# Optimization experiments

Hardware: AMD Instinct MI355X
Metric: run time of the kernel (lower is better)

The kernel has to match this reference:

```python
import jax, jax.numpy as jnp
import numpy as np

B, T, C = 4, 2048, 1024
N_HEAD = 16
HEAD_DIM = C // N_HEAD


def setup_inputs() -> dict:
    key = jax.random.key(0)
    ks = jax.random.split(key, 5)
    s = 0.02
    return {
        "x": jax.random.normal(ks[0], (B, T, C), dtype=jnp.float32),
        "w_attn": jax.random.normal(ks[1], (C, 3 * C), dtype=jnp.float32) * s,
        "b_attn": jnp.zeros((3 * C,), dtype=jnp.float32),
        "w_proj": jax.random.normal(ks[2], (C, C), dtype=jnp.float32) * s,
        "b_proj": jnp.zeros((C,), dtype=jnp.float32),
    }


def reference(x, w_attn, b_attn, w_proj, b_proj):
    Bx, Tx, Cx = x.shape
    qkv = x @ w_attn + b_attn  # [B,T,3C]
    q, k, v = jnp.split(qkv, 3, axis=-1)
    # [B, H, T, D]
    q = q.reshape(Bx, Tx, N_HEAD, HEAD_DIM).transpose(0, 2, 1, 3)
    k = k.reshape(Bx, Tx, N_HEAD, HEAD_DIM).transpose(0, 2, 1, 3)
    v = v.reshape(Bx, Tx, N_HEAD, HEAD_DIM).transpose(0, 2, 1, 3)
    scale = 1.0 / np.sqrt(HEAD_DIM).astype(np.float32)
    att = jnp.einsum("bhqd,bhkd->bhqk", q, k) * scale  # [B,H,T,T]
    causal = jnp.tril(jnp.ones((Tx, Tx), dtype=bool))
    att = jnp.where(causal[None, None], att, jnp.float32(-jnp.inf))
    att = jax.nn.softmax(att, axis=-1)
    y = jnp.einsum("bhqk,bhkd->bhqd", att, v)  # [B,H,T,D]
    y = y.transpose(0, 2, 1, 3).reshape(Bx, Tx, Cx)
    return y @ w_proj + b_proj
```

## Files before the change

### kernel.cpp

```cpp
#include <hip/hip_runtime.h>
#include <hip/hip_bf16.h>

#define T_SEQ 2048
#define NHEAD 16
#define HDIM  64
#define CDIM  1024

typedef __attribute__((ext_vector_type(8))) short bf16x8;
typedef __attribute__((ext_vector_type(4))) short bf16x4;
typedef __attribute__((ext_vector_type(4))) float f32x4;

__device__ __forceinline__ unsigned short f2bf(float f) {
  union { __hip_bfloat16 h; unsigned short u; } c;
  c.h = __float2bfloat16(f);
  return c.u;
}

#define GLD16(g, l) __builtin_amdgcn_global_load_lds( \
  (const __attribute__((address_space(1))) void*)(g), \
  (__attribute__((address_space(3))) void*)(l), 16, 0, 0)

__global__ void cvt_bf16(const float* __restrict__ in, unsigned short* __restrict__ out, int n4) {
  const int i = blockIdx.x * 256 + threadIdx.x;
  if (i >= n4) return;
  const float4 v = ((const float4*)in)[i];
  ushort4 o;
  o.x = f2bf(v.x); o.y = f2bf(v.y); o.z = f2bf(v.z); o.w = f2bf(v.w);
  ((ushort4*)out)[i] = o;
}

__global__ void transpose_cvt(const float* __restrict__ in, unsigned short* __restrict__ out,
                              int R, int C) {
  __shared__ float tile[32][33];
  const int tx = threadIdx.x & 31, ty = threadIdx.x >> 5;
  const int c0 = blockIdx.x * 32, r0 = blockIdx.y * 32;
#pragma unroll
  for (int i = 0; i < 32; i += 8)
    tile[ty + i][tx] = in[(size_t)(r0 + ty + i) * C + c0 + tx];
  __syncthreads();
#pragma unroll
  for (int i = 0; i < 32; i += 8)
    out[(size_t)(c0 + ty + i) * R + r0 + tx] = f2bf(tile[tx][ty + i]);
}

template<int OUTF32>
__global__ __launch_bounds__(256, 2)
void gemm_bt(const unsigned short* __restrict__ A, const unsigned short* __restrict__ BT,
             const float* __restrict__ bias, void* __restrict__ outp,
             int M, int N, int K) {
  const int tid = threadIdx.x;
  const int w = tid >> 6, lane = tid & 63;
  const int lg = lane >> 4, l15 = lane & 15;
  const int wr = w >> 1, wc = w & 1;
  const int n0 = blockIdx.x * 128, m0 = blockIdx.y * 128;

  __shared__ unsigned short As[128 * 32];
  __shared__ unsigned short Bs[128 * 32];

  f32x4 acc[4][4] = {};

  for (int k0 = 0; k0 < K; k0 += 32) {
    __syncthreads();
#pragma unroll
    for (int i = 0; i < 2; ++i) {
      const int cb = i * 256 + w * 64;
      const int c  = cb + lane;
      const int row = c >> 2, slot = c & 3;
      GLD16(A  + (size_t)(m0 + row) * K + k0 + slot * 8, (char*)As + cb * 16);
      GLD16(BT + (size_t)(n0 + row) * K + k0 + slot * 8, (char*)Bs + cb * 16);
    }
    __syncthreads();
    bf16x8 af[4], bfr[4];
#pragma unroll
    for (int mt = 0; mt < 4; ++mt)
      af[mt] = *(const bf16x8*)&As[(wr * 64 + mt * 16 + l15) * 32 + lg * 8];
#pragma unroll
    for (int nt = 0; nt < 4; ++nt)
      bfr[nt] = *(const bf16x8*)&Bs[(wc * 64 + nt * 16 + l15) * 32 + lg * 8];
#pragma unroll
    for (int mt = 0; mt < 4; ++mt)
#pragma unroll
      for (int nt = 0; nt < 4; ++nt)
        acc[mt][nt] = __builtin_amdgcn_mfma_f32_16x16x32_bf16(af[mt], bfr[nt], acc[mt][nt], 0, 0, 0);
  }

#pragma unroll
  for (int mt = 0; mt < 4; ++mt) {
#pragma unroll
    for (int nt = 0; nt < 4; ++nt) {
      const int col = n0 + wc * 64 + nt * 16 + l15;
      const float bv = bias[col];
#pragma unroll
      for (int j = 0; j < 4; ++j) {
        const int row = m0 + wr * 64 + mt * 16 + lg * 4 + j;
        const float v = acc[mt][nt][j] + bv;
        if (OUTF32) ((float*)outp)[(size_t)row * N + col] = v;
        else ((unsigned short*)outp)[(size_t)row * N + col] = f2bf(v);
      }
    }
  }
}

#define EXPC 0.18033688f
__global__ __launch_bounds__(512, 4)
void attn_causal4(const unsigned short* __restrict__ qkv, unsigned short* __restrict__ att) {
  const int tid = threadIdx.x;
  const int w = tid >> 6, lane = tid & 63;
  const int lg = lane >> 4, l15 = lane & 15;

  const int fid = blockIdx.x;
  const int f2 = (fid & 7) * 64 + (fid >> 3);
  const int pair = f2 & 7, bh = f2 >> 3;
  const int b = bh >> 4, h = bh & 15;

  __shared__ unsigned short Kl[2][2][64][32];
  __shared__ unsigned short Vt[2][64][64];
  __shared__ unsigned short Pl[8][16][64];

  const unsigned short* base = qkv + (size_t)b * T_SEQ * 3072;

  auto STAGE_K = [&](int kv0, int buf) {
    const int c = tid;
    const int kc = c >> 8, kv = (c >> 2) & 63;
    const int s2 = (c & 3) ^ ((kv >> 1) & 3);
    GLD16(base + (size_t)(kv0 + kv) * 3072 + 1024 + h * 64 + kc * 32 + s2 * 8,
          (char*)&Kl[buf][0][0][0] + w * 1024);
  };

  bf16x4 vra, vrb;
  const int vkp = tid >> 4, vd4 = tid & 15;
  auto VLOAD = [&](int kv0) {
    const unsigned short* p = base + (size_t)(kv0 + 2 * vkp) * 3072 + 2048 + h * 64 + vd4 * 4;
    vra = *(const bf16x4*)p;
    vrb = *(const bf16x4*)(p + 3072);
  };
  auto VWRITE = [&](int buf) {
    const int ch = vkp >> 2, cl = (vkp & 3) * 2;
#pragma unroll
    for (int j = 0; j < 4; ++j) {
      const int r = vd4 * 4 + j;
      const unsigned int u = (unsigned short)vra[j] |
                             ((unsigned int)(unsigned short)vrb[j] << 16);
      *(unsigned int*)&Vt[buf][r][((ch ^ (r >> 3) ^ (r & 7)) << 3) + cl] = u;
    }
  };

  for (int half = 0; half < 2; ++half) {
    const int qt = half ? (15 - pair) : pair;
    const int q0 = qt << 7;
    const int ntl = (qt + 1) << 1;
    const int qmin = q0 + w * 16;
    const int qme = qmin + l15;

    bf16x8 qf[2];
#pragma unroll
    for (int kc = 0; kc < 2; ++kc)
      qf[kc] = *(const bf16x8*)(base + (size_t)qme * 3072 + h * 64 + kc * 32 + lg * 8);

    f32x4 oacc[4] = {};
    float m = -1e30f, l = 0.f;

    STAGE_K(0, 0);
    VLOAD(0);
    VWRITE(0);
    __syncthreads();

    for (int t = 0; t < ntl; ++t) {
      const int cur = t & 1, nxt = cur ^ 1;
      const bool pf = (t + 1) < ntl;
      if (pf) { STAGE_K((t + 1) << 6, nxt); VLOAD((t + 1) << 6); }
      const int kv0 = t << 6;
      const bool skip = kv0 > qmin + 15;

      if (!skip) {
        const int ksl = (lg ^ ((l15 >> 1) & 3)) * 8;
        f32x4 sc[4];
#pragma unroll
        for (int kg = 0; kg < 4; ++kg) {
          f32x4 s = {};
#pragma unroll
          for (int kc = 0; kc < 2; ++kc) {
            bf16x8 kf = *(const bf16x8*)&Kl[cur][kc][kg * 16 + l15][ksl];
            s = __builtin_amdgcn_mfma_f32_16x16x32_bf16(kf, qf[kc], s, 0, 0, 0);
          }
          sc[kg] = s;
        }

        const bool needmask = (kv0 + 63 > qmin);
        float sv[4][4];
        float mx = -1e30f;
#pragma unroll
        for (int kg = 0; kg < 4; ++kg)
#pragma unroll
          for (int j = 0; j < 4; ++j) {
            float s = sc[kg][j];
            if (needmask && (kv0 + kg * 16 + lg * 4 + j > qme)) s = -1e30f;
            sv[kg][j] = s;
            mx = fmaxf(mx, s);
          }

        if (__any(mx > m + 55.4f)) {
          float mw = fmaxf(mx, __shfl_xor(mx, 16));
          mw = fmaxf(mw, __shfl_xor(mw, 32));
          const float mnew = fmaxf(m, mw);
          const float alc = exp2f((m - mnew) * EXPC);
          m = mnew;
          l *= alc;
          float alq[4];
#pragma unroll
          for (int j = 0; j < 4; ++j)
            alq[j] = __shfl(alc, (lane & 48) | (lg * 4 + j));
#pragma unroll
          for (int dt = 0; dt < 4; ++dt)
#pragma unroll
            for (int j = 0; j < 4; ++j) oacc[dt][j] *= alq[j];
        }

        const float mc = m * EXPC;
        float rs = 0.f;
#pragma unroll
        for (int kg = 0; kg < 4; ++kg) {
          ushort4 pw;
          float p0 = exp2f(__fmaf_rn(sv[kg][0], EXPC, -mc));
          float p1 = exp2f(__fmaf_rn(sv[kg][1], EXPC, -mc));
          float p2 = exp2f(__fmaf_rn(sv[kg][2], EXPC, -mc));
          float p3 = exp2f(__fmaf_rn(sv[kg][3], EXPC, -mc));
          rs += (p0 + p1) + (p2 + p3);
          pw.x = f2bf(p0); pw.y = f2bf(p1); pw.z = f2bf(p2); pw.w = f2bf(p3);
          const int slot = (kg * 2 + (lg >> 1)) ^ (l15 & 7);
          *(ushort4*)&Pl[w][l15][slot * 8 + (lg & 1) * 4] = pw;
        }
        rs += __shfl_xor(rs, 16);
        rs += __shfl_xor(rs, 32);
        l += rs;
      }

      asm volatile("s_waitcnt lgkmcnt(0)" ::: "memory");
      __builtin_amdgcn_sched_barrier(0);

      if (!skip) {
        bf16x8 pa[2];
#pragma unroll
        for (int ks = 0; ks < 2; ++ks)
          pa[ks] = *(const bf16x8*)&Pl[w][l15][((ks * 4 + lg) ^ (l15 & 7)) * 8];
#pragma unroll
        for (int dt = 0; dt < 4; ++dt) {
          f32x4 o = oacc[dt];
          const int d = dt * 16 + l15;
          const int gx = (d >> 3) ^ (d & 7);
#pragma unroll
          for (int ks = 0; ks < 2; ++ks) {
            bf16x8 vb = *(const bf16x8*)&Vt[cur][d][((ks * 4 + lg) ^ gx) << 3];
            o = __builtin_amdgcn_mfma_f32_16x16x32_bf16(pa[ks], vb, o, 0, 0, 0);
          }
          oacc[dt] = o;
        }
      }

      if (pf) VWRITE(nxt);
      __syncthreads();
    }

    float lq[4];
#pragma unroll
    for (int j = 0; j < 4; ++j)
      lq[j] = __shfl(l, (lane & 48) | (lg * 4 + j));
#pragma unroll
    for (int dt = 0; dt < 4; ++dt)
#pragma unroll
      for (int j = 0; j < 4; ++j) {
        const int q = qmin + lg * 4 + j;
        att[(size_t)(b * T_SEQ + q) * CDIM + h * HDIM + dt * 16 + l15] =
            f2bf(oacc[dt][j] / lq[j]);
      }
  }
}

extern "C" void kernel_launch(void* const* d_in, const int* in_sizes, int n_in,
                              void* d_out, int out_size, void* d_ws, size_t ws_size,
                              hipStream_t stream) {
  const float* x      = (const float*)d_in[0];
  const float* w_attn = (const float*)d_in[1];
  const float* b_attn = (const float*)d_in[2];
  const float* w_proj = (const float*)d_in[3];
  const float* b_proj = (const float*)d_in[4];

  char* ws = (char*)d_ws;
  unsigned short* xb  = (unsigned short*)(ws + 0);
  unsigned short* wat = (unsigned short*)(ws + 16777216);
  unsigned short* wpt = (unsigned short*)(ws + 23068672);
  unsigned short* qkv = (unsigned short*)(ws + 25165824);
  unsigned short* att = (unsigned short*)(ws + 75497472);

  cvt_bf16<<<8192, 256, 0, stream>>>(x, xb, 2097152);
  transpose_cvt<<<dim3(96, 32), 256, 0, stream>>>(w_attn, wat, 1024, 3072);
  transpose_cvt<<<dim3(32, 32), 256, 0, stream>>>(w_proj, wpt, 1024, 1024);
  gemm_bt<0><<<dim3(24, 64), 256, 0, stream>>>(xb, wat, b_attn, (void*)qkv, 8192, 3072, 1024);
  attn_causal4<<<dim3(512), 512, 0, stream>>>(qkv, att);
  gemm_bt<1><<<dim3(8, 64), 256, 0, stream>>>(att, wpt, b_proj, d_out, 8192, 1024, 1024);
}
```

Measured before the change: 202.9 us.

## Keep softmax probabilities in registers via permuted K rows, row sums by MFMA

The K staging now loads rows in a permuted order, so the S-accumulator layout produced by the QK MFMA directly matches the A-operand layout of the PV MFMA. This removes the per-tile LDS round trip for P (store, wait, reload). The row sums are now computed with MFMAs against a ones vector instead of cross-lane shuffles. The change also adds setprio hints around the MFMA sections and makes the query base wave-uniform via readfirstlane. The cost is two extra MFMAs per tile and a trickier permutation that must stay consistent with the causal-mask column indices.

```diff
diff --git a/kernel.cpp b/kernel.cpp
--- a/kernel.cpp
+++ b/kernel.cpp
@@ -103,7 +103,7 @@
 
 #define EXPC 0.18033688f
 __global__ __launch_bounds__(512, 4)
-void attn_causal4(const unsigned short* __restrict__ qkv, unsigned short* __restrict__ att) {
+void attn_causal5(const unsigned short* __restrict__ qkv, unsigned short* __restrict__ att) {
   const int tid = threadIdx.x;
   const int w = tid >> 6, lane = tid & 63;
   const int lg = lane >> 4, l15 = lane & 15;
@@ -115,15 +115,15 @@
 
   __shared__ unsigned short Kl[2][2][64][32];
   __shared__ unsigned short Vt[2][64][64];
-  __shared__ unsigned short Pl[8][16][64];
 
   const unsigned short* base = qkv + (size_t)b * T_SEQ * 3072;
 
   auto STAGE_K = [&](int kv0, int buf) {
     const int c = tid;
-    const int kc = c >> 8, kv = (c >> 2) & 63;
-    const int s2 = (c & 3) ^ ((kv >> 1) & 3);
-    GLD16(base + (size_t)(kv0 + kv) * 3072 + 1024 + h * 64 + kc * 32 + s2 * 8,
+    const int kc = c >> 8, slot = (c >> 2) & 63;
+    const int s2 = (c & 3) ^ ((slot >> 1) & 3);
+    const int v = (slot & 35) | ((slot & 8) << 1) | ((slot & 4) << 1) | ((slot & 16) >> 2);
+    GLD16(base + (size_t)(kv0 + v) * 3072 + 1024 + h * 64 + kc * 32 + s2 * 8,
           (char*)&Kl[buf][0][0][0] + w * 1024);
   };
 
@@ -145,12 +145,16 @@
     }
   };
 
+  bf16x8 ones;
+#pragma unroll
+  for (int j = 0; j < 8; ++j) ones[j] = (short)0x3F80;
+
   for (int half = 0; half < 2; ++half) {
     const int qt = half ? (15 - pair) : pair;
     const int q0 = qt << 7;
     const int ntl = (qt + 1) << 1;
-    const int qmin = q0 + w * 16;
-    const int qme = qmin + l15;
+    const int qminS = __builtin_amdgcn_readfirstlane(q0 + w * 16);
+    const int qme = qminS + l15;
 
     bf16x8 qf[2];
 #pragma unroll
@@ -158,7 +162,8 @@
       qf[kc] = *(const bf16x8*)(base + (size_t)qme * 3072 + h * 64 + kc * 32 + lg * 8);
 
     f32x4 oacc[4] = {};
-    float m = -1e30f, l = 0.f;
+    f32x4 lsum = {};
+    float m = -1e30f;
 
     STAGE_K(0, 0);
     VLOAD(0);
@@ -170,11 +175,11 @@
       const bool pf = (t + 1) < ntl;
       if (pf) { STAGE_K((t + 1) << 6, nxt); VLOAD((t + 1) << 6); }
       const int kv0 = t << 6;
-      const bool skip = kv0 > qmin + 15;
-
-      if (!skip) {
+
+      if (kv0 <= qminS + 15) {
         const int ksl = (lg ^ ((l15 >> 1) & 3)) * 8;
         f32x4 sc[4];
+        __builtin_amdgcn_s_setprio(1);
 #pragma unroll
         for (int kg = 0; kg < 4; ++kg) {
           f32x4 s = {};
@@ -185,19 +190,31 @@
           }
           sc[kg] = s;
         }
-
-        const bool needmask = (kv0 + 63 > qmin);
+        __builtin_amdgcn_s_setprio(0);
+
         float sv[4][4];
+        if (kv0 + 63 > qminS) {
+#pragma unroll
+          for (int kg = 0; kg < 4; ++kg) {
+            const int colb = kv0 + ((kg >> 1) << 5) + ((kg & 1) << 2) + lg * 8;
+#pragma unroll
+            for (int j = 0; j < 4; ++j)
+              sv[kg][j] = (colb + j <= qme) ? sc[kg][j] : -1e30f;
+          }
+        } else {
+#pragma unroll
+          for (int kg = 0; kg < 4; ++kg)
+#pragma unroll
+            for (int j = 0; j < 4; ++j) sv[kg][j] = sc[kg][j];
+        }
+
         float mx = -1e30f;
 #pragma unroll
-        for (int kg = 0; kg < 4; ++kg)
-#pragma unroll
-          for (int j = 0; j < 4; ++j) {
-            float s = sc[kg][j];
-            if (needmask && (kv0 + kg * 16 + lg * 4 + j > qme)) s = -1e30f;
-            sv[kg][j] = s;
-            mx = fmaxf(mx, s);
-          }
+        for (int kg = 0; kg < 4; ++kg) {
+          const float a = fmaxf(sv[kg][0], sv[kg][1]);
+          const float c2 = fmaxf(sv[kg][2], sv[kg][3]);
+          mx = fmaxf(mx, fmaxf(a, c2));
+        }
 
         if (__any(mx > m + 55.4f)) {
           float mw = fmaxf(mx, __shfl_xor(mx, 16));
@@ -205,44 +222,33 @@
           const float mnew = fmaxf(m, mw);
           const float alc = exp2f((m - mnew) * EXPC);
           m = mnew;
-          l *= alc;
           float alq[4];
 #pragma unroll
           for (int j = 0; j < 4; ++j)
             alq[j] = __shfl(alc, (lane & 48) | (lg * 4 + j));
 #pragma unroll
-          for (int dt = 0; dt < 4; ++dt)
-#pragma unroll
-            for (int j = 0; j < 4; ++j) oacc[dt][j] *= alq[j];
+          for (int j = 0; j < 4; ++j) {
+            lsum[j] *= alq[j];
+#pragma unroll
+            for (int dt = 0; dt < 4; ++dt) oacc[dt][j] *= alq[j];
+          }
         }
 
         const float mc = m * EXPC;
-        float rs = 0.f;
+        bf16x8 pa[2];
 #pragma unroll
         for (int kg = 0; kg < 4; ++kg) {
-          ushort4 pw;
-          float p0 = exp2f(__fmaf_rn(sv[kg][0], EXPC, -mc));
-          float p1 = exp2f(__fmaf_rn(sv[kg][1], EXPC, -mc));
-          float p2 = exp2f(__fmaf_rn(sv[kg][2], EXPC, -mc));
-          float p3 = exp2f(__fmaf_rn(sv[kg][3], EXPC, -mc));
-          rs += (p0 + p1) + (p2 + p3);
-          pw.x = f2bf(p0); pw.y = f2bf(p1); pw.z = f2bf(p2); pw.w = f2bf(p3);
-          const int slot = (kg * 2 + (lg >> 1)) ^ (l15 & 7);
-          *(ushort4*)&Pl[w][l15][slot * 8 + (lg & 1) * 4] = pw;
-        }
-        rs += __shfl_xor(rs, 16);
-        rs += __shfl_xor(rs, 32);
-        l += rs;
-      }
-
-      asm volatile("s_waitcnt lgkmcnt(0)" ::: "memory");
-      __builtin_amdgcn_sched_barrier(0);
-
-      if (!skip) {
-        bf16x8 pa[2];
-#pragma unroll
-        for (int ks = 0; ks < 2; ++ks)
-          pa[ks] = *(const bf16x8*)&Pl[w][l15][((ks * 4 + lg) ^ (l15 & 7)) * 8];
+          const int ks = kg >> 1, off = (kg & 1) * 4;
+#pragma unroll
+          for (int j = 0; j < 4; ++j) {
+            const float p = exp2f(__fmaf_rn(sv[kg][j], EXPC, -mc));
+            pa[ks][off + j] = (short)f2bf(p);
+          }
+        }
+
+        __builtin_amdgcn_s_setprio(1);
+        lsum = __builtin_amdgcn_mfma_f32_16x16x32_bf16(pa[0], ones, lsum, 0, 0, 0);
+        lsum = __builtin_amdgcn_mfma_f32_16x16x32_bf16(pa[1], ones, lsum, 0, 0, 0);
 #pragma unroll
         for (int dt = 0; dt < 4; ++dt) {
           f32x4 o = oacc[dt];
@@ -255,23 +261,20 @@
           }
           oacc[dt] = o;
         }
+        __builtin_amdgcn_s_setprio(0);
       }
 
       if (pf) VWRITE(nxt);
       __syncthreads();
     }
 
-    float lq[4];
-#pragma unroll
-    for (int j = 0; j < 4; ++j)
-      lq[j] = __shfl(l, (lane & 48) | (lg * 4 + j));
 #pragma unroll
     for (int dt = 0; dt < 4; ++dt)
 #pragma unroll
       for (int j = 0; j < 4; ++j) {
-        const int q = qmin + lg * 4 + j;
+        const int q = qminS + lg * 4 + j;
         att[(size_t)(b * T_SEQ + q) * CDIM + h * HDIM + dt * 16 + l15] =
-            f2bf(oacc[dt][j] / lq[j]);
+            f2bf(oacc[dt][j] / lsum[j]);
       }
   }
 }
@@ -296,6 +299,6 @@
   transpose_cvt<<<dim3(96, 32), 256, 0, stream>>>(w_attn, wat, 1024, 3072);
   transpose_cvt<<<dim3(32, 32), 256, 0, stream>>>(w_proj, wpt, 1024, 1024);
   gemm_bt<0><<<dim3(24, 64), 256, 0, stream>>>(xb, wat, b_attn, (void*)qkv, 8192, 3072, 1024);
-  attn_causal4<<<dim3(512), 512, 0, stream>>>(qkv, att);
+  attn_causal5<<<dim3(512), 512, 0, stream>>>(qkv, att);
   gemm_bt<1><<<dim3(8, 64), 256, 0, stream>>>(att, wpt, b_proj, d_out, 8192, 1024, 1024);
 }
```

New measurement: 187.6 us. -7.5%, faster.
